# Kernel optimization log

Measured on AMD Instinct MI355X. Metric: run time of the kernel, lower is better.

The kernel has to match this reference:

```python
import jax, jax.numpy as jnp
import numpy as np

D_MODEL = 2048
NUM_HEADS = 16
D_K = D_MODEL // NUM_HEADS


def setup_inputs() -> dict:
    key = jax.random.key(0)
    ks = jax.random.split(key, 9)
    s = 1.0 / np.sqrt(D_MODEL)
    return {
        "x": jax.random.normal(ks[0], (2, 2048, D_MODEL), dtype=jnp.float32),
        "Wq": jax.random.normal(ks[1], (D_MODEL, D_MODEL), dtype=jnp.float32) * s,
        "bq": jax.random.normal(ks[2], (D_MODEL,), dtype=jnp.float32) * 0.01,
        "Wk": jax.random.normal(ks[3], (D_MODEL, D_MODEL), dtype=jnp.float32) * s,
        "bk": jax.random.normal(ks[4], (D_MODEL,), dtype=jnp.float32) * 0.01,
        "Wv": jax.random.normal(ks[5], (D_MODEL, D_MODEL), dtype=jnp.float32) * s,
        "bv": jax.random.normal(ks[6], (D_MODEL,), dtype=jnp.float32) * 0.01,
        "Wo": jax.random.normal(ks[7], (D_MODEL, D_MODEL), dtype=jnp.float32) * s,
        "bo": jax.random.normal(ks[8], (D_MODEL,), dtype=jnp.float32) * 0.01,
    }


def reference(x, Wq, bq, Wk, bk, Wv, bv, Wo, bo):
    B, T, C = x.shape
    H, Dk = NUM_HEADS, D_K
    # projections (torch Linear: y = x @ W^T + b; here weights stored as [in,out])
    q = (x @ Wq + bq).reshape(B, T, H, Dk).transpose(0, 2, 1, 3)  # [B,H,T,Dk]
    k = (x @ Wk + bk).reshape(B, T, H, Dk).transpose(0, 2, 1, 3)
    v = (x @ Wv + bv).reshape(B, T, H, Dk).transpose(0, 2, 1, 3)
    score = jnp.einsum("bhqd,bhkd->bhqk", q, k) / jnp.sqrt(jnp.float32(Dk))
    attn = jax.nn.softmax(score, axis=-1)
    out = jnp.einsum("bhqk,bhkd->bhqd", attn, v)  # [B,H,T,Dk]
    out = out.transpose(0, 2, 1, 3).reshape(B, T, C)
    return out @ Wo + bo
```

## Files before the change

### kernel.cpp

```cpp
#include <hip/hip_runtime.h>
#include <cstdint>

typedef _Float16 f16;
typedef __attribute__((ext_vector_type(4))) _Float16 f16x4;
typedef __attribute__((ext_vector_type(8))) _Float16 f16x8;
typedef __attribute__((ext_vector_type(4))) float f32x4;

#define DM   2048
#define TSEQ 2048
#define NB   2
#define NH   16
#define DKH  128
#define LOG2E 1.44269504088896f

__device__ __forceinline__ void gload_lds16(const void* g, void* l) {
  __builtin_amdgcn_global_load_lds((const __attribute__((address_space(1))) void*)g,
                                   (__attribute__((address_space(3))) void*)l, 16, 0, 0);
}

#define SBAR()  asm volatile("s_barrier" ::: "memory")
#define LGKM0() { asm volatile("s_waitcnt lgkmcnt(0)" ::: "memory"); __builtin_amdgcn_sched_barrier(0); }

__global__ __launch_bounds__(256) void cvt_kernel(const float* __restrict__ src,
                                                  f16* __restrict__ dst, int n8) {
  int i = blockIdx.x * 256 + threadIdx.x;
  if (i >= n8) return;
  const float4* s = (const float4*)src + 2 * (size_t)i;
  float4 a = s[0], b = s[1];
  f16x8 o;
  o[0]=(f16)a.x; o[1]=(f16)a.y; o[2]=(f16)a.z; o[3]=(f16)a.w;
  o[4]=(f16)b.x; o[5]=(f16)b.y; o[6]=(f16)b.z; o[7]=(f16)b.w;
  ((f16x8*)dst)[i] = o;
}

__global__ __launch_bounds__(256) void wt_kernel(const float* __restrict__ W0, const float* __restrict__ W1,
                                                 const float* __restrict__ W2, const float* __restrict__ W3,
                                                 f16* __restrict__ Dqkv, f16* __restrict__ Dout) {
  __shared__ f16 S[64 * 80];
  int z = blockIdx.z;
  const float* W = (z == 0) ? W0 : (z == 1) ? W1 : (z == 2) ? W2 : W3;
  f16* D = (z < 3) ? (Dqkv + (size_t)z * DM * DM) : Dout;
  int n0 = blockIdx.x * 64, k0 = blockIdx.y * 64;
  int tid = threadIdx.x;
#pragma unroll
  for (int i = 0; i < 4; i++) {
    int flat = i * 256 + tid;
    int r = flat >> 4, c4 = flat & 15;
    float4 v = *(const float4*)(W + (size_t)(k0 + r) * DM + n0 + c4 * 4);
    S[(c4 * 4 + 0) * 80 + r] = (f16)v.x;
    S[(c4 * 4 + 1) * 80 + r] = (f16)v.y;
    S[(c4 * 4 + 2) * 80 + r] = (f16)v.z;
    S[(c4 * 4 + 3) * 80 + r] = (f16)v.w;
  }
  __syncthreads();
#pragma unroll
  for (int i = 0; i < 2; i++) {
    int flat = i * 256 + tid;
    int nl = flat >> 3, kc = flat & 7;
    f16x8 v = *(const f16x8*)&S[nl * 80 + kc * 8];
    *(f16x8*)(D + (size_t)(n0 + nl) * DM + k0 + kc * 8) = v;
  }
}

template <int MODE>
__global__ __launch_bounds__(512, 2) void gemm_kernel(const f16* __restrict__ A, const f16* __restrict__ Bt,
                                                      const float* __restrict__ b0, const float* __restrict__ b1,
                                                      const float* __restrict__ b2,
                                                      f16* __restrict__ Oh, float* __restrict__ Of) {
  __shared__ __align__(16) f16 As[2][256 * 64];
  __shared__ __align__(16) f16 Bs[2][128 * 64];
  const int K = DM;
  const int NT = K / 64;
  const int NITER = NT / 2;
  const int NXB = (MODE == 0) ? 48 : 16;
  const int CPX = (MODE == 0) ? 96 : 32;
  int tid = threadIdx.x, l = tid & 63, w = tid >> 6;
  int lo = l & 15, hi = l >> 4;
  int wm = w >> 1, wn = w & 1;
  int lin = blockIdx.x;
  int swz = (lin & 7) * CPX + (lin >> 3);
  int bx = swz % NXB, by = swz / NXB;
  int m0 = by * 256, n0 = bx * 128;

  const f16* Ag = A + (size_t)m0 * K;
  const f16* Bg = Bt + (size_t)n0 * K;

  auto stageA = [&](int b, int h, int t) {
#pragma unroll
    for (int i = 0; i < 2; i++) {
      int flat = i * 512 + tid;
      int row = flat >> 3, c = flat & 7;
      int csw = c ^ (row & 7);
      gload_lds16(Ag + (size_t)(h * 128 + row) * K + t * 64 + csw * 8,
                  &As[b][h * 8192 + i * 4096 + w * 512]);
    }
  };
  auto stageB = [&](int b, int t) {
#pragma unroll
    for (int i = 0; i < 2; i++) {
      int flat = i * 512 + tid;
      int row = flat >> 3, c = flat & 7;
      int csw = c ^ (row & 7);
      gload_lds16(Bg + (size_t)row * K + t * 64 + csw * 8,
                  &Bs[b][i * 4096 + w * 512]);
    }
  };

  f32x4 acc[4][4] = {};
  f16x8 bfr[4][2];

#define READ_BFRAGS(b)                                                          \
  {                                                                             \
    _Pragma("unroll")                                                           \
    for (int ni = 0; ni < 4; ni++) {                                            \
      int row = wn * 64 + ni * 16 + lo;                                         \
      bfr[ni][0] = *(const f16x8*)&Bs[b][row * 64 + (((0 + hi) ^ (row & 7)) << 3)]; \
      bfr[ni][1] = *(const f16x8*)&Bs[b][row * 64 + (((4 + hi) ^ (row & 7)) << 3)]; \
    }                                                                           \
  }

#define PHASE_HEAD(bq, q)                                                       \
    f16x8 af0, af1;                                                             \
    {                                                                           \
      int row = wm * 64 + (q) * 16 + lo;                                        \
      af0 = *(const f16x8*)&As[bq][row * 64 + (((0 + hi) ^ (row & 7)) << 3)];   \
      af1 = *(const f16x8*)&As[bq][row * 64 + (((4 + hi) ^ (row & 7)) << 3)];   \
    }

#define PHASE_MFMA(q)                                                           \
    __builtin_amdgcn_s_setprio(1);                                              \
    _Pragma("unroll")                                                           \
    for (int ni = 0; ni < 4; ni++) {                                            \
      acc[q][ni] = __builtin_amdgcn_mfma_f32_16x16x32_f16(af0, bfr[ni][0], acc[q][ni], 0, 0, 0); \
      acc[q][ni] = __builtin_amdgcn_mfma_f32_16x16x32_f16(af1, bfr[ni][1], acc[q][ni], 0, 0, 0); \
    }                                                                           \
    __builtin_amdgcn_s_setprio(0);

  stageB(0, 0);
  stageA(0, 0, 0);
  stageA(0, 1, 0);
  stageB(1, 1);
  asm volatile("s_waitcnt vmcnt(2)" ::: "memory");
  SBAR();

#pragma unroll 1
  for (int it = 0; it < NITER; ++it) {
    int t1  = 2 * it + 1;
    int tn0 = (2 * it + 2 < NT) ? 2 * it + 2 : NT - 1;
    int tn1 = (2 * it + 3 < NT) ? 2 * it + 3 : NT - 1;

    {
      READ_BFRAGS(0);
      PHASE_HEAD(0, 0);
      stageA(1, 0, t1);
      asm volatile("s_waitcnt lgkmcnt(8)" ::: "memory");
      SBAR(); LGKM0(); PHASE_MFMA(0); SBAR();
    }
    {
      PHASE_HEAD(0, 1);
      stageA(1, 1, t1);
      SBAR(); LGKM0(); PHASE_MFMA(1); SBAR();
    }
    {
      PHASE_HEAD(0, 2);
      stageB(0, tn0);
      SBAR(); LGKM0(); PHASE_MFMA(2); SBAR();
    }
    {
      PHASE_HEAD(0, 3);
      SBAR(); LGKM0(); PHASE_MFMA(3);
      asm volatile("s_waitcnt vmcnt(2)" ::: "memory");
      SBAR();
    }
    {
      READ_BFRAGS(1);
      PHASE_HEAD(1, 0);
      stageA(0, 0, tn0);
      asm volatile("s_waitcnt lgkmcnt(8)" ::: "memory");
      SBAR(); LGKM0(); PHASE_MFMA(0); SBAR();
    }
    {
      PHASE_HEAD(1, 1);
      stageA(0, 1, tn0);
      SBAR(); LGKM0(); PHASE_MFMA(1); SBAR();
    }
    {
      PHASE_HEAD(1, 2);
      stageB(1, tn1);
      SBAR(); LGKM0(); PHASE_MFMA(2); SBAR();
    }
    {
      PHASE_HEAD(1, 3);
      SBAR(); LGKM0(); PHASE_MFMA(3);
      asm volatile("s_waitcnt vmcnt(2)" ::: "memory");
      SBAR();
    }
  }

#pragma unroll
  for (int mi = 0; mi < 4; mi++) {
    int gm = m0 + wm * 64 + mi * 16 + ((l >> 4) << 2);
#pragma unroll
    for (int ni = 0; ni < 4; ni++) {
      int gn = n0 + wn * 64 + ni * 16 + (l & 15);
      if (MODE == 0) {
        int proj = gn >> 11, nn = gn & 2047;
        const float* bp = (proj == 0) ? b0 : (proj == 1) ? b1 : b2;
        float bias = bp[nn];
        int h = nn >> 7, d = nn & 127;
        int b = gm >> 11;
        int t0 = gm & 2047;
        if (proj < 2) {
#pragma unroll
          for (int r = 0; r < 4; r++) {
            Oh[(size_t)proj * ((size_t)NB * NH * TSEQ * DKH) +
               (((size_t)(b * NH + h) * TSEQ + t0 + r) * DKH) + d] = (f16)(acc[mi][ni][r] + bias);
          }
        } else {
          f16x4 pk;
#pragma unroll
          for (int r = 0; r < 4; r++) pk[r] = (f16)(acc[mi][ni][r] + bias);
          *(f16x4*)(Oh + 2ull * ((size_t)NB * NH * TSEQ * DKH) +
                    ((size_t)(b * NH + h) * DKH + d) * TSEQ + t0) = pk;
        }
      } else {
        float bias = b0[gn];
#pragma unroll
        for (int r = 0; r < 4; r++)
          Of[(size_t)(gm + r) * DM + gn] = acc[mi][ni][r] + bias;
      }
    }
  }
  asm volatile("s_waitcnt vmcnt(0)" ::: "memory");
#undef READ_BFRAGS
#undef PHASE_HEAD
#undef PHASE_MFMA
}

__global__ __launch_bounds__(256, 2) void attn_kernel(const f16* __restrict__ Qb, const f16* __restrict__ Kb,
                                                      const f16* __restrict__ Vtb, f16* __restrict__ AO) {
  __shared__ f16 Ks[64 * 128];
  __shared__ f16 Vt[128 * 64];
  __shared__ f16 Ps[4][32 * 72];
  int tid = threadIdx.x, l = tid & 63, w = tid >> 6;
  int lo = l & 15, hi = l >> 4;
  int lin = blockIdx.x;
  int xcd = lin & 7, slot = lin >> 3;
  int bh = xcd * 4 + (slot & 3), qt = slot >> 2;
  const float CSC = 0.12753257f;
  const float THR = 62.0f;
  const f16* Qg = Qb + (size_t)bh * TSEQ * DKH;
  const f16* Kg = Kb + (size_t)bh * TSEQ * DKH;
  const f16* Vg = Vtb + (size_t)bh * DKH * TSEQ;

  f16x8 aq[2][4];
#pragma unroll
  for (int hf = 0; hf < 2; hf++) {
    int qrow = qt * 128 + w * 32 + hf * 16 + lo;
#pragma unroll
    for (int c = 0; c < 4; c++)
      aq[hf][c] = *(const f16x8*)(Qg + (size_t)qrow * DKH + c * 32 + (hi << 3));
  }

  f32x4 o[2][8] = {};
  float mrow[2] = {-INFINITY, -INFINITY};
  float lrow[2] = {0.f, 0.f};

  for (int ktile = 0; ktile < TSEQ / 64; ++ktile) {
    __syncthreads();
#pragma unroll
    for (int i = 0; i < 4; i++) {
      int chunk = (w * 4 + i) * 64 + l;
      int rowk = chunk >> 4, c = chunk & 15;
      int csw = c ^ (rowk & 15);
      gload_lds16(Kg + (size_t)(ktile * 64 + rowk) * DKH + csw * 8, &Ks[(w * 4 + i) * 512]);
    }
#pragma unroll
    for (int i = 0; i < 4; i++) {
      int chunk = (w * 4 + i) * 64 + l;
      int d = chunk >> 3, c = chunk & 7;
      int csw = c ^ (d & 7);
      gload_lds16(Vg + (size_t)d * TSEQ + ktile * 64 + csw * 8, &Vt[(w * 4 + i) * 512]);
    }
    __syncthreads();

    f32x4 s[2][4] = {};
    __builtin_amdgcn_s_setprio(1);
#pragma unroll
    for (int ks = 0; ks < 4; ++ks) {
      int ktl = ks * 16 + lo;
#pragma unroll
      for (int c = 0; c < 4; c++) {
        int cc = (c * 4 + hi) ^ lo;
        f16x8 bk = *(const f16x8*)&Ks[ktl * 128 + cc * 8];
        s[0][ks] = __builtin_amdgcn_mfma_f32_16x16x32_f16(bk, aq[0][c], s[0][ks], 0, 0, 0);
        s[1][ks] = __builtin_amdgcn_mfma_f32_16x16x32_f16(bk, aq[1][c], s[1][ks], 0, 0, 0);
      }
    }
    __builtin_amdgcn_s_setprio(0);

#pragma unroll
    for (int hf = 0; hf < 2; hf++) {
      float mk[4];
#pragma unroll
      for (int ks = 0; ks < 4; ks++)
        mk[ks] = fmaxf(fmaxf(s[hf][ks][0], s[hf][ks][1]), fmaxf(s[hf][ks][2], s[hf][ks][3]));
      float mt = fmaxf(fmaxf(mk[0], mk[1]), fmaxf(mk[2], mk[3]));
      mt = fmaxf(mt, __shfl_xor(mt, 16));
      mt = fmaxf(mt, __shfl_xor(mt, 32));

      if (__any(mt > mrow[hf] + THR)) {
        float mn = fmaxf(mrow[hf], mt);
        float al = exp2f((mrow[hf] - mn) * CSC);
        mrow[hf] = mn;
        lrow[hf] *= al;
        float alr[4];
#pragma unroll
        for (int r = 0; r < 4; r++) alr[r] = __shfl(al, (hi << 2) + r);
#pragma unroll
        for (int dsub = 0; dsub < 8; dsub++)
#pragma unroll
          for (int r = 0; r < 4; r++) o[hf][dsub][r] *= alr[r];
      }

      float mCn = -mrow[hf] * CSC;
      float sum = 0.f;
#pragma unroll
      for (int ks = 0; ks < 4; ks++) {
        f16x4 pk;
        float part = 0.f;
#pragma unroll
        for (int r = 0; r < 4; r++) {
          float p = exp2f(__builtin_fmaf(s[hf][ks][r], CSC, mCn));
          pk[r] = (f16)p;
          part += p;
        }
        sum += part;
        *(f16x4*)&Ps[w][(hf * 16 + lo) * 72 + ks * 16 + (hi << 2)] = pk;
      }
      sum += __shfl_xor(sum, 16);
      sum += __shfl_xor(sum, 32);
      lrow[hf] += sum;
    }

    f16x8 pa[2][2];
#pragma unroll
    for (int hf = 0; hf < 2; hf++)
#pragma unroll
      for (int kk = 0; kk < 2; kk++)
        pa[hf][kk] = *(const f16x8*)&Ps[w][(hf * 16 + lo) * 72 + kk * 32 + (hi << 3)];
    __builtin_amdgcn_s_setprio(1);
#pragma unroll
    for (int kk = 0; kk < 2; kk++) {
#pragma unroll
      for (int dsub = 0; dsub < 8; dsub++) {
        int d = dsub * 16 + lo;
        f16x8 vf = *(const f16x8*)&Vt[d * 64 + (((kk * 4 + hi) ^ (d & 7)) << 3)];
        o[0][dsub] = __builtin_amdgcn_mfma_f32_16x16x32_f16(pa[0][kk], vf, o[0][dsub], 0, 0, 0);
        o[1][dsub] = __builtin_amdgcn_mfma_f32_16x16x32_f16(pa[1][kk], vf, o[1][dsub], 0, 0, 0);
      }
    }
    __builtin_amdgcn_s_setprio(0);
  }

  int b = bh >> 4, h = bh & 15;
#pragma unroll
  for (int hf = 0; hf < 2; hf++) {
    float inv = 1.0f / lrow[hf];
    float invr[4];
#pragma unroll
    for (int r = 0; r < 4; r++) invr[r] = __shfl(inv, (hi << 2) + r);
#pragma unroll
    for (int r = 0; r < 4; r++) {
      int t = qt * 128 + w * 32 + hf * 16 + (hi << 2) + r;
      f16* dst = AO + ((size_t)b * TSEQ + t) * DM + h * DKH;
#pragma unroll
      for (int dsub = 0; dsub < 8; dsub++)
        dst[dsub * 16 + lo] = (f16)(o[hf][dsub][r] * invr[r]);
    }
  }
}

extern "C" void kernel_launch(void* const* d_in, const int* in_sizes, int n_in,
                              void* d_out, int out_size, void* d_ws, size_t ws_size,
                              hipStream_t stream) {
  const float* x  = (const float*)d_in[0];
  const float* Wq = (const float*)d_in[1];
  const float* bq = (const float*)d_in[2];
  const float* Wk = (const float*)d_in[3];
  const float* bk = (const float*)d_in[4];
  const float* Wv = (const float*)d_in[5];
  const float* bv = (const float*)d_in[6];
  const float* Wo = (const float*)d_in[7];
  const float* bo = (const float*)d_in[8];

  f16* ws    = (f16*)d_ws;
  f16* xb    = ws;
  f16* WtQKV = ws + 8388608ull;
  f16* WtO   = ws + 20971520ull;
  f16* Q     = ws + 25165824ull;
  f16* Kp    = ws + 33554432ull;
  f16* Vp    = ws + 41943040ull;
  f16* AO    = xb;

  cvt_kernel<<<4096, 256, 0, stream>>>(x, xb, (NB * TSEQ * DM) / 8);
  wt_kernel<<<dim3(32, 32, 4), 256, 0, stream>>>(Wq, Wk, Wv, Wo, WtQKV, WtO);
  gemm_kernel<0><<<768, 512, 0, stream>>>(xb, WtQKV, bq, bk, bv, Q, nullptr);
  attn_kernel<<<512, 256, 0, stream>>>(Q, Kp, Vp, AO);
  gemm_kernel<1><<<256, 512, 0, stream>>>(AO, WtO, bo, nullptr, nullptr, nullptr, (float*)d_out);
}
```

Measured before the change: 290.2 us.

## Enlarge GEMM block tile to 256x256 with 2x4 wave layout

The GEMM block tile grows from 256x128 to 256x256. Each of the 8 waves now computes a 128x64 sub-tile with 32 accumulators, and the B staging buffer is doubled and loaded in two halves, with the pipeline waits adjusted to match. The aim is to raise arithmetic intensity and cut redundant global and LDS traffic per FLOP. The cost is about 128KB of LDS per block, which limits each CU to one resident block. The grid also shrinks to 384 blocks for the QKV GEMM and 128 blocks for the output projection, which can leave many CUs idle.

```diff
diff --git a/kernel.cpp b/kernel.cpp
--- a/kernel.cpp
+++ b/kernel.cpp
@@ -18,8 +18,10 @@
                                    (__attribute__((address_space(3))) void*)l, 16, 0, 0);
 }
 
-#define SBAR()  asm volatile("s_barrier" ::: "memory")
-#define LGKM0() { asm volatile("s_waitcnt lgkmcnt(0)" ::: "memory"); __builtin_amdgcn_sched_barrier(0); }
+#define SBAR()   asm volatile("s_barrier" ::: "memory")
+#define LGKM0()  { asm volatile("s_waitcnt lgkmcnt(0)" ::: "memory"); __builtin_amdgcn_sched_barrier(0); }
+#define LGKM8()  asm volatile("s_waitcnt lgkmcnt(8)" ::: "memory")
+#define VMCNT4() asm volatile("s_waitcnt vmcnt(4)" ::: "memory")
 
 __global__ __launch_bounds__(256) void cvt_kernel(const float* __restrict__ src,
                                                   f16* __restrict__ dst, int n8) {
@@ -68,19 +70,18 @@
                                                       const float* __restrict__ b2,
                                                       f16* __restrict__ Oh, float* __restrict__ Of) {
   __shared__ __align__(16) f16 As[2][256 * 64];
-  __shared__ __align__(16) f16 Bs[2][128 * 64];
+  __shared__ __align__(16) f16 Bs[2][256 * 64];
   const int K = DM;
   const int NT = K / 64;
   const int NITER = NT / 2;
-  const int NXB = (MODE == 0) ? 48 : 16;
-  const int CPX = (MODE == 0) ? 96 : 32;
+  constexpr int CPX = (MODE == 0) ? 48 : 16;
   int tid = threadIdx.x, l = tid & 63, w = tid >> 6;
   int lo = l & 15, hi = l >> 4;
-  int wm = w >> 1, wn = w & 1;
+  int wm = w >> 2, wn = w & 3;
   int lin = blockIdx.x;
   int swz = (lin & 7) * CPX + (lin >> 3);
-  int bx = swz % NXB, by = swz / NXB;
-  int m0 = by * 256, n0 = bx * 128;
+  int by = swz & 15, bx = swz >> 4;
+  int m0 = by * 256, n0 = bx * 256;
 
   const f16* Ag = A + (size_t)m0 * K;
   const f16* Bg = Bt + (size_t)n0 * K;
@@ -95,114 +96,118 @@
                   &As[b][h * 8192 + i * 4096 + w * 512]);
     }
   };
-  auto stageB = [&](int b, int t) {
+  auto stageB = [&](int b, int h, int t) {
 #pragma unroll
     for (int i = 0; i < 2; i++) {
       int flat = i * 512 + tid;
       int row = flat >> 3, c = flat & 7;
       int csw = c ^ (row & 7);
-      gload_lds16(Bg + (size_t)row * K + t * 64 + csw * 8,
-                  &Bs[b][i * 4096 + w * 512]);
+      gload_lds16(Bg + (size_t)(h * 128 + row) * K + t * 64 + csw * 8,
+                  &Bs[b][h * 8192 + i * 4096 + w * 512]);
     }
   };
 
-  f32x4 acc[4][4] = {};
+  f32x4 acc[8][4] = {};
   f16x8 bfr[4][2];
-
-#define READ_BFRAGS(b)                                                          \
-  {                                                                             \
-    _Pragma("unroll")                                                           \
-    for (int ni = 0; ni < 4; ni++) {                                            \
-      int row = wn * 64 + ni * 16 + lo;                                         \
+  f16x8 af[2][2];
+
+#define READ_BFRAGS(b)                                                              \
+  {                                                                                 \
+    _Pragma("unroll")                                                               \
+    for (int ni = 0; ni < 4; ni++) {                                                \
+      int row = wn * 64 + ni * 16 + lo;                                             \
       bfr[ni][0] = *(const f16x8*)&Bs[b][row * 64 + (((0 + hi) ^ (row & 7)) << 3)]; \
       bfr[ni][1] = *(const f16x8*)&Bs[b][row * 64 + (((4 + hi) ^ (row & 7)) << 3)]; \
-    }                                                                           \
-  }
-
-#define PHASE_HEAD(bq, q)                                                       \
-    f16x8 af0, af1;                                                             \
-    {                                                                           \
-      int row = wm * 64 + (q) * 16 + lo;                                        \
-      af0 = *(const f16x8*)&As[bq][row * 64 + (((0 + hi) ^ (row & 7)) << 3)];   \
-      af1 = *(const f16x8*)&As[bq][row * 64 + (((4 + hi) ^ (row & 7)) << 3)];   \
-    }
-
-#define PHASE_MFMA(q)                                                           \
-    __builtin_amdgcn_s_setprio(1);                                              \
-    _Pragma("unroll")                                                           \
-    for (int ni = 0; ni < 4; ni++) {                                            \
-      acc[q][ni] = __builtin_amdgcn_mfma_f32_16x16x32_f16(af0, bfr[ni][0], acc[q][ni], 0, 0, 0); \
-      acc[q][ni] = __builtin_amdgcn_mfma_f32_16x16x32_f16(af1, bfr[ni][1], acc[q][ni], 0, 0, 0); \
-    }                                                                           \
+    }                                                                               \
+  }
+
+#define READ_AFRAGS(b, q)                                                           \
+  {                                                                                 \
+    _Pragma("unroll")                                                               \
+    for (int e = 0; e < 2; e++) {                                                   \
+      int row = wm * 128 + ((q) * 2 + e) * 16 + lo;                                 \
+      af[e][0] = *(const f16x8*)&As[b][row * 64 + (((0 + hi) ^ (row & 7)) << 3)];   \
+      af[e][1] = *(const f16x8*)&As[b][row * 64 + (((4 + hi) ^ (row & 7)) << 3)];   \
+    }                                                                               \
+  }
+
+#define MFMA_Q(q)                                                                   \
+    __builtin_amdgcn_s_setprio(1);                                                  \
+    _Pragma("unroll")                                                               \
+    for (int e = 0; e < 2; e++)                                                     \
+      _Pragma("unroll")                                                             \
+      for (int ni = 0; ni < 4; ni++) {                                              \
+        acc[(q)*2+e][ni] = __builtin_amdgcn_mfma_f32_16x16x32_f16(af[e][0], bfr[ni][0], acc[(q)*2+e][ni], 0, 0, 0); \
+        acc[(q)*2+e][ni] = __builtin_amdgcn_mfma_f32_16x16x32_f16(af[e][1], bfr[ni][1], acc[(q)*2+e][ni], 0, 0, 0); \
+      }                                                                             \
     __builtin_amdgcn_s_setprio(0);
 
-  stageB(0, 0);
-  stageA(0, 0, 0);
-  stageA(0, 1, 0);
-  stageB(1, 1);
-  asm volatile("s_waitcnt vmcnt(2)" ::: "memory");
+  stageB(0, 0, 0); stageB(0, 1, 0);
+  stageA(0, 0, 0); stageA(0, 1, 0);
+  stageB(1, 0, 1); stageB(1, 1, 1);
+  VMCNT4();
   SBAR();
 
 #pragma unroll 1
   for (int it = 0; it < NITER; ++it) {
-    int t1  = 2 * it + 1;
-    int tn0 = (2 * it + 2 < NT) ? 2 * it + 2 : NT - 1;
-    int tn1 = (2 * it + 3 < NT) ? 2 * it + 3 : NT - 1;
-
-    {
-      READ_BFRAGS(0);
-      PHASE_HEAD(0, 0);
-      stageA(1, 0, t1);
-      asm volatile("s_waitcnt lgkmcnt(8)" ::: "memory");
-      SBAR(); LGKM0(); PHASE_MFMA(0); SBAR();
-    }
-    {
-      PHASE_HEAD(0, 1);
-      stageA(1, 1, t1);
-      SBAR(); LGKM0(); PHASE_MFMA(1); SBAR();
-    }
-    {
-      PHASE_HEAD(0, 2);
-      stageB(0, tn0);
-      SBAR(); LGKM0(); PHASE_MFMA(2); SBAR();
-    }
-    {
-      PHASE_HEAD(0, 3);
-      SBAR(); LGKM0(); PHASE_MFMA(3);
-      asm volatile("s_waitcnt vmcnt(2)" ::: "memory");
+    int T1 = 2 * it + 1;
+    int t2 = (2 * it + 2 < NT) ? 2 * it + 2 : NT - 1;
+    int t3 = (2 * it + 3 < NT) ? 2 * it + 3 : NT - 1;
+
+    {
+      READ_BFRAGS(0); READ_AFRAGS(0, 0);
+      stageA(1, 0, T1);
+      LGKM8();
+      SBAR(); LGKM0(); MFMA_Q(0); SBAR();
+    }
+    {
+      READ_AFRAGS(0, 1);
+      stageA(1, 1, T1); stageB(0, 0, t2);
+      SBAR(); LGKM0(); MFMA_Q(1); SBAR();
+    }
+    {
+      READ_AFRAGS(0, 2);
+      stageB(0, 1, t2);
+      SBAR(); LGKM0(); MFMA_Q(2); SBAR();
+    }
+    {
+      READ_AFRAGS(0, 3);
+      SBAR(); LGKM0(); MFMA_Q(3);
+      VMCNT4();
       SBAR();
     }
     {
-      READ_BFRAGS(1);
-      PHASE_HEAD(1, 0);
-      stageA(0, 0, tn0);
-      asm volatile("s_waitcnt lgkmcnt(8)" ::: "memory");
-      SBAR(); LGKM0(); PHASE_MFMA(0); SBAR();
-    }
-    {
-      PHASE_HEAD(1, 1);
-      stageA(0, 1, tn0);
-      SBAR(); LGKM0(); PHASE_MFMA(1); SBAR();
-    }
-    {
-      PHASE_HEAD(1, 2);
-      stageB(1, tn1);
-      SBAR(); LGKM0(); PHASE_MFMA(2); SBAR();
-    }
-    {
-      PHASE_HEAD(1, 3);
-      SBAR(); LGKM0(); PHASE_MFMA(3);
-      asm volatile("s_waitcnt vmcnt(2)" ::: "memory");
+      READ_BFRAGS(1); READ_AFRAGS(1, 0);
+      stageA(0, 0, t2);
+      LGKM8();
+      SBAR(); LGKM0(); MFMA_Q(0); SBAR();
+    }
+    {
+      READ_AFRAGS(1, 1);
+      stageA(0, 1, t2);
+      SBAR(); LGKM0(); MFMA_Q(1); SBAR();
+    }
+    {
+      READ_AFRAGS(1, 2);
+      stageB(1, 0, t3);
+      SBAR(); LGKM0(); MFMA_Q(2); SBAR();
+    }
+    {
+      READ_AFRAGS(1, 3);
+      stageB(1, 1, t3);
+      SBAR(); LGKM0(); MFMA_Q(3);
+      VMCNT4();
       SBAR();
     }
   }
-
-#pragma unroll
-  for (int mi = 0; mi < 4; mi++) {
-    int gm = m0 + wm * 64 + mi * 16 + ((l >> 4) << 2);
+  asm volatile("s_waitcnt vmcnt(0)" ::: "memory");
+
+#pragma unroll
+  for (int mi = 0; mi < 8; mi++) {
+    int gm = m0 + wm * 128 + mi * 16 + (hi << 2);
 #pragma unroll
     for (int ni = 0; ni < 4; ni++) {
-      int gn = n0 + wn * 64 + ni * 16 + (l & 15);
+      int gn = n0 + wn * 64 + ni * 16 + lo;
       if (MODE == 0) {
         int proj = gn >> 11, nn = gn & 2047;
         const float* bp = (proj == 0) ? b0 : (proj == 1) ? b1 : b2;
@@ -231,10 +236,9 @@
       }
     }
   }
-  asm volatile("s_waitcnt vmcnt(0)" ::: "memory");
 #undef READ_BFRAGS
-#undef PHASE_HEAD
-#undef PHASE_MFMA
+#undef READ_AFRAGS
+#undef MFMA_Q
 }
 
 __global__ __launch_bounds__(256, 2) void attn_kernel(const f16* __restrict__ Qb, const f16* __restrict__ Kb,
@@ -405,7 +409,7 @@
 
   cvt_kernel<<<4096, 256, 0, stream>>>(x, xb, (NB * TSEQ * DM) / 8);
   wt_kernel<<<dim3(32, 32, 4), 256, 0, stream>>>(Wq, Wk, Wv, Wo, WtQKV, WtO);
-  gemm_kernel<0><<<768, 512, 0, stream>>>(xb, WtQKV, bq, bk, bv, Q, nullptr);
+  gemm_kernel<0><<<384, 512, 0, stream>>>(xb, WtQKV, bq, bk, bv, Q, nullptr);
   attn_kernel<<<512, 256, 0, stream>>>(Q, Kp, Vp, AO);
-  gemm_kernel<1><<<256, 512, 0, stream>>>(AO, WtO, bo, nullptr, nullptr, nullptr, (float*)d_out);
-}
+  gemm_kernel<1><<<128, 512, 0, stream>>>(AO, WtO, bo, nullptr, nullptr, nullptr, (float*)d_out);
+}
```

Result: slower. 300.6 us (+3.6%).
